# Kernel tuning notes

Hardware: AMD Instinct MI355X
Metric: run time of the kernel (lower is better)

Reference implementation:

```python
import jax, jax.numpy as jnp
import numpy as np


def reference(x, weight, bias):
    """Per-sample dynamic conv2d, expressed as one grouped convolution.

    x:      (B, C_in, H, W)
    weight: (B, C_out, C_in, kH, kW)
    bias:   (B, C_out)
    returns (B, C_out, H_out, W_out) with H_out = H - kH + 1 (valid conv)
    """
    B, C_in, H, W = x.shape
    C_out, kH, kW = weight.shape[1], weight.shape[3], weight.shape[4]
    # Fold batch into channels: groups=B grouped conv == B independent convs.
    x_g = x.reshape(1, B * C_in, H, W)
    w_g = weight.reshape(B * C_out, C_in, kH, kW)
    out = jax.lax.conv_general_dilated(
        x_g, w_g,
        window_strides=(1, 1),
        padding='VALID',
        dimension_numbers=('NCHW', 'OIHW', 'NCHW'),
        feature_group_count=B,
    )  # (1, B*C_out, H_out, W_out)
    out = out.reshape(B, C_out, out.shape[2], out.shape[3])
    return out + bias[:, :, None, None]


def setup_inputs() -> dict:
    key = jax.random.key(0)
    k1, k2, k3 = jax.random.split(key, 3)
    B, C_in, C_out, H, W, kH, kW = 16, 64, 64, 128, 128, 3, 3
    x = jax.random.normal(k1, (B, C_in, H, W), dtype=jnp.float32)
    weight = jax.random.normal(k2, (B, C_out, C_in, kH, kW), dtype=jnp.float32) * 0.05
    bias = jax.random.normal(k3, (B, C_out), dtype=jnp.float32)
    return {"x": x, "weight": weight, "bias": bias}
```

## Files before the change

kernel.cpp:

```cpp
#include <hip/hip_runtime.h>
#include <hip/hip_bf16.h>

#define BATCH 16
#define CI 64
#define CO 64
#define H 128
#define W 128
#define HO 126
#define WO 126
#define HW (H * W)

typedef short bfrag __attribute__((ext_vector_type(8)));
typedef float ffrag __attribute__((ext_vector_type(4)));

static __device__ __forceinline__ unsigned short f2bf(float f) {
    unsigned u = __float_as_uint(f);
    u += 0x7fffu + ((u >> 16) & 1u);
    return (unsigned short)(u >> 16);
}

__global__ void wt_prepass(const float* __restrict__ w, unsigned short* __restrict__ w_t) {
    int i = blockIdx.x * 256 + threadIdx.x;
    int ci = i & 63;
    int co = (i >> 6) & 63;
    int bs = i >> 12;
    int b = bs / 9, s = bs - b * 9;
    w_t[i] = f2bf(w[(((b * 64 + co) * 64 + ci) * 9) + s]);
}

static __device__ __forceinline__ void stage_write(unsigned short* __restrict__ slabp,
                                                   const float4* __restrict__ v,
                                                   int st_o, int st_cg) {
    #pragma unroll
    for (int k = 0; k < 4; ++k) {
        const int col = st_cg * 4 + k;
        unsigned int u[4];
        #pragma unroll
        for (int e = 0; e < 4; ++e) {
            __hip_bfloat162 h2 = __float22bfloat162_rn(make_float2(
                ((const float*)&v[2 * e])[k], ((const float*)&v[2 * e + 1])[k]));
            u[e] = *(unsigned int*)&h2;
        }
        *(uint4*)&slabp[(col * 8 + (st_o ^ (col & 7))) * 8] = *(const uint4*)u;
    }
}

__launch_bounds__(512, 2)
__global__ void dynconv_fused(const float* __restrict__ x,
                              const unsigned short* __restrict__ w_t,
                              const float* __restrict__ bias,
                              float* __restrict__ out) {
    __shared__ __align__(16) unsigned short xs[6 * 8192];

    const int tid = threadIdx.x;
    const int gx  = blockIdx.x;
    const int b   = blockIdx.y;
    const int nunits = (gx == 15) ? 3 : 4;
    const int y00 = gx * 8;

    const int wave = tid >> 6, lane = tid & 63;
    const int l16 = lane & 15, lq = lane >> 4;
    const int wm = wave & 3;
    const int wn = wave >> 2;

    const int st_o  = tid & 7;
    const int st_cg = (tid >> 3) & 31;
    const int st_r  = tid >> 8;

    const float* stp = x + (size_t)b * CI * HW + (size_t)(st_o * 8) * HW + st_cg * 4;

    const bfrag* wtb = (const bfrag*)w_t + (size_t)(b * 9) * 512;
    const int co_b = wm * 16 + l16;
    bfrag a[9][2];
    #pragma unroll
    for (int s = 0; s < 9; ++s)
        #pragma unroll
        for (int ks = 0; ks < 2; ++ks)
            a[s][ks] = wtb[s * 512 + co_b * 8 + ks * 4 + lq];

    float bv[4];
    #pragma unroll
    for (int r = 0; r < 4; ++r)
        bv[r] = bias[b * 64 + wm * 16 + lq * 4 + r];

    {
        float4 v0[8], v1[8];
        const float* p0 = stp + (size_t)(y00 + st_r) * W;
        const float* p1 = stp + (size_t)(y00 + 2 + st_r) * W;
        #pragma unroll
        for (int e = 0; e < 8; ++e) v0[e] = *(const float4*)(p0 + (size_t)e * HW);
        #pragma unroll
        for (int e = 0; e < 8; ++e) v1[e] = *(const float4*)(p1 + (size_t)e * HW);
        stage_write(&xs[(st_r) * 8192], v0, st_o, st_cg);
        stage_write(&xs[(2 + st_r) * 8192], v1, st_o, st_cg);
    }
    asm volatile("s_waitcnt lgkmcnt(0)" ::: "memory");
    __builtin_amdgcn_s_barrier();
    __builtin_amdgcn_sched_barrier(0);

    for (int j = 0; j < nunits; ++j) {
        const bool hn = (j + 1) < nunits;
        const int u2j = 2 * j;

        float4 v[8];
        if (hn) {
            const float* p = stp + (size_t)(y00 + u2j + 4 + st_r) * W;
            #pragma unroll
            for (int e = 0; e < 8; ++e) v[e] = *(const float4*)(p + (size_t)e * HW);
        }

        ffrag acc[8];
        #pragma unroll
        for (int nt = 0; nt < 8; ++nt) acc[nt] = (ffrag){0.f, 0.f, 0.f, 0.f};

        #pragma unroll
        for (int s = 0; s < 9; ++s) {
            const int dy = s / 3, dx = s - dy * 3;
            int t = u2j + wn + dy;
            if (t >= 6) t -= 6;
            const unsigned short* slabp = &xs[t * 8192];
            #pragma unroll
            for (int ks = 0; ks < 2; ++ks) {
                const int o = ks * 4 + lq;
                #pragma unroll
                for (int nt = 0; nt < 8; ++nt) {
                    int colx = nt * 16 + l16 + dx;
                    if (colx > 127) colx = 127;
                    const bfrag bf = *(const bfrag*)&slabp[(colx * 8 + (o ^ (colx & 7))) * 8];
                    acc[nt] = __builtin_amdgcn_mfma_f32_16x16x32_bf16(a[s][ks], bf, acc[nt], 0, 0, 0);
                }
            }
        }

        if (hn) {
            int t = u2j + 4 + st_r;
            if (t >= 6) t -= 6;
            stage_write(&xs[t * 8192], v, st_o, st_cg);
            asm volatile("s_waitcnt lgkmcnt(0)" ::: "memory");
            __builtin_amdgcn_s_barrier();
            __builtin_amdgcn_sched_barrier(0);
        }

        const int oy = y00 + u2j + wn;
        #pragma unroll
        for (int r = 0; r < 4; ++r) {
            float* op = out + ((size_t)(b * 64 + wm * 16 + lq * 4 + r) * HO + oy) * WO;
            const float bvv = bv[r];
            #pragma unroll
            for (int nt = 0; nt < 8; ++nt) {
                const int ox = nt * 16 + l16;
                if (ox < WO) op[ox] = acc[nt][r] + bvv;
            }
        }
    }
}

extern "C" void kernel_launch(void* const* d_in, const int* in_sizes, int n_in,
                              void* d_out, int out_size, void* d_ws, size_t ws_size,
                              hipStream_t stream) {
    const float* x    = (const float*)d_in[0];
    const float* w    = (const float*)d_in[1];
    const float* bias = (const float*)d_in[2];
    float* out        = (float*)d_out;

    unsigned short* w_t = (unsigned short*)d_ws;

    wt_prepass<<<dim3(589824 / 256), dim3(256), 0, stream>>>(w, w_t);
    dynconv_fused<<<dim3(16, BATCH), dim3(512), 0, stream>>>(x, w_t, bias, out);
}
```

Measured before the change: 138.0 us.

## Shrink conv blocks to 4 waves with one output row per step

Blocks drop from 512 to 256 threads, and each block covers 4 output rows instead of 8. The grid doubles to 32x16, and the shared-memory ring shrinks from 6 to 4 slabs. All waves now share the same output row and each handles 16 output channels, so each iteration stages one input row instead of two. The goal is more blocks and better occupancy and load balance. The cost is more halo re-reads of input rows across blocks and more barriers per output row. A sched_barrier is also added after the prefetch loads.

```diff
diff --git a/kernel.cpp b/kernel.cpp
--- a/kernel.cpp
+++ b/kernel.cpp
@@ -45,32 +45,29 @@
     }
 }
 
-__launch_bounds__(512, 2)
+__launch_bounds__(256, 2)
 __global__ void dynconv_fused(const float* __restrict__ x,
                               const unsigned short* __restrict__ w_t,
                               const float* __restrict__ bias,
                               float* __restrict__ out) {
-    __shared__ __align__(16) unsigned short xs[6 * 8192];
+    __shared__ __align__(16) unsigned short xs[4 * 8192];
 
     const int tid = threadIdx.x;
     const int gx  = blockIdx.x;
     const int b   = blockIdx.y;
-    const int nunits = (gx == 15) ? 3 : 4;
-    const int y00 = gx * 8;
+    const int y0  = gx * 4;
+    const int nunits = (gx == 31) ? 2 : 4;
 
     const int wave = tid >> 6, lane = tid & 63;
     const int l16 = lane & 15, lq = lane >> 4;
-    const int wm = wave & 3;
-    const int wn = wave >> 2;
 
     const int st_o  = tid & 7;
-    const int st_cg = (tid >> 3) & 31;
-    const int st_r  = tid >> 8;
+    const int st_cg = tid >> 3;
 
     const float* stp = x + (size_t)b * CI * HW + (size_t)(st_o * 8) * HW + st_cg * 4;
 
     const bfrag* wtb = (const bfrag*)w_t + (size_t)(b * 9) * 512;
-    const int co_b = wm * 16 + l16;
+    const int co_b = wave * 16 + l16;
     bfrag a[9][2];
     #pragma unroll
     for (int s = 0; s < 9; ++s)
@@ -81,18 +78,19 @@
     float bv[4];
     #pragma unroll
     for (int r = 0; r < 4; ++r)
-        bv[r] = bias[b * 64 + wm * 16 + lq * 4 + r];
+        bv[r] = bias[b * 64 + wave * 16 + lq * 4 + r];
 
     {
-        float4 v0[8], v1[8];
-        const float* p0 = stp + (size_t)(y00 + st_r) * W;
-        const float* p1 = stp + (size_t)(y00 + 2 + st_r) * W;
+        float4 v[3][8];
         #pragma unroll
-        for (int e = 0; e < 8; ++e) v0[e] = *(const float4*)(p0 + (size_t)e * HW);
+        for (int rr = 0; rr < 3; ++rr) {
+            const float* p = stp + (size_t)(y0 + rr) * W;
+            #pragma unroll
+            for (int e = 0; e < 8; ++e) v[rr][e] = *(const float4*)(p + (size_t)e * HW);
+        }
         #pragma unroll
-        for (int e = 0; e < 8; ++e) v1[e] = *(const float4*)(p1 + (size_t)e * HW);
-        stage_write(&xs[(st_r) * 8192], v0, st_o, st_cg);
-        stage_write(&xs[(2 + st_r) * 8192], v1, st_o, st_cg);
+        for (int rr = 0; rr < 3; ++rr)
+            stage_write(&xs[rr * 8192], v[rr], st_o, st_cg);
     }
     asm volatile("s_waitcnt lgkmcnt(0)" ::: "memory");
     __builtin_amdgcn_s_barrier();
@@ -100,14 +98,14 @@
 
     for (int j = 0; j < nunits; ++j) {
         const bool hn = (j + 1) < nunits;
-        const int u2j = 2 * j;
 
         float4 v[8];
         if (hn) {
-            const float* p = stp + (size_t)(y00 + u2j + 4 + st_r) * W;
+            const float* p = stp + (size_t)(y0 + j + 3) * W;
             #pragma unroll
             for (int e = 0; e < 8; ++e) v[e] = *(const float4*)(p + (size_t)e * HW);
         }
+        __builtin_amdgcn_sched_barrier(0);
 
         ffrag acc[8];
         #pragma unroll
@@ -116,9 +114,7 @@
         #pragma unroll
         for (int s = 0; s < 9; ++s) {
             const int dy = s / 3, dx = s - dy * 3;
-            int t = u2j + wn + dy;
-            if (t >= 6) t -= 6;
-            const unsigned short* slabp = &xs[t * 8192];
+            const unsigned short* slabp = &xs[((j + dy) & 3) * 8192];
             #pragma unroll
             for (int ks = 0; ks < 2; ++ks) {
                 const int o = ks * 4 + lq;
@@ -133,18 +129,16 @@
         }
 
         if (hn) {
-            int t = u2j + 4 + st_r;
-            if (t >= 6) t -= 6;
-            stage_write(&xs[t * 8192], v, st_o, st_cg);
+            stage_write(&xs[((j + 3) & 3) * 8192], v, st_o, st_cg);
             asm volatile("s_waitcnt lgkmcnt(0)" ::: "memory");
             __builtin_amdgcn_s_barrier();
             __builtin_amdgcn_sched_barrier(0);
         }
 
-        const int oy = y00 + u2j + wn;
+        const int oy = y0 + j;
         #pragma unroll
         for (int r = 0; r < 4; ++r) {
-            float* op = out + ((size_t)(b * 64 + wm * 16 + lq * 4 + r) * HO + oy) * WO;
+            float* op = out + ((size_t)(b * 64 + wave * 16 + lq * 4 + r) * HO + oy) * WO;
             const float bvv = bv[r];
             #pragma unroll
             for (int nt = 0; nt < 8; ++nt) {
@@ -166,5 +160,5 @@
     unsigned short* w_t = (unsigned short*)d_ws;
 
     wt_prepass<<<dim3(589824 / 256), dim3(256), 0, stream>>>(w, w_t);
-    dynconv_fused<<<dim3(16, BATCH), dim3(512), 0, stream>>>(x, w_t, bias, out);
+    dynconv_fused<<<dim3(32, BATCH), dim3(256), 0, stream>>>(x, w_t, bias, out);
 }
```

Measured after the change: 134.2 us. -2.8%, faster.
